# Performance work log

Measured on AMD Instinct MI355X. Metric: run time of the kernel, lower is better.

## Reference

```python
import jax, jax.numpy as jnp
import numpy as np

NUM_HEADS = 16
EPS = 1e-6
ROPE_BASE = 10000.0

def _thw(N, TT):
    table = {2640: (3, 22, 40), 1530: (3, 17, 30), 6120: (3, 34, 60), 660: (3, 11, 20)}
    return table.get(N - TT, (3, 23, 40))

def _positions(t, h, w):
    tt, hh, ww = np.meshgrid(np.arange(t), np.arange(h), np.arange(w), indexing='ij')
    return jnp.asarray(np.stack([tt, hh, ww], -1).reshape(-1, 3), jnp.float32)  # (THW, 3)

def _rope1d(x, pos):
    # x: (B,H,T,d) one axis-chunk, pos: (T,) positions for that axis
    d = x.shape[-1]
    inv_freq = 1.0 / (ROPE_BASE ** (jnp.arange(0, d, 2, dtype=jnp.float32) / d))
    ang = pos[:, None] * inv_freq                     # (T, d/2)
    cos = jnp.concatenate([jnp.cos(ang)] * 2, -1)     # (T, d)
    sin = jnp.concatenate([jnp.sin(ang)] * 2, -1)
    x1, x2 = x[..., : d // 2], x[..., d // 2:]
    return x * cos + jnp.concatenate([-x2, x1], -1) * sin

def _rope3d(x, pos, TT):
    # first TT tokens (text) pass through; video tokens get per-axis rotation
    pre, vid = x[:, :, :TT], x[:, :, TT:]
    chunks = jnp.split(vid, 3, axis=-1)               # t/h/w axis chunks
    rot = [_rope1d(c, pos[:, i]) for i, c in enumerate(chunks)]
    return jnp.concatenate([pre, jnp.concatenate(rot, -1)], axis=2)

def _rms(x, w):
    return x * jax.lax.rsqrt(jnp.mean(x * x, -1, keepdims=True) + EPS) * w

def setup_inputs() -> dict:
    key = jax.random.key(0)
    ks = jax.random.split(key, 12)
    B, N, C = 1, 2866, 1536
    Dh = C // NUM_HEADS
    s = 0.02
    return {
        'x': jax.random.normal(ks[0], (B, N, C), jnp.float32),
        'Wq': jax.random.normal(ks[1], (C, C), jnp.float32) * s,
        'bq': jnp.zeros((C,), jnp.float32),
        'Wk': jax.random.normal(ks[2], (C, C), jnp.float32) * s,
        'bk': jnp.zeros((C,), jnp.float32),
        'Wv': jax.random.normal(ks[3], (C, C), jnp.float32) * s,
        'bv': jnp.zeros((C,), jnp.float32),
        'qn_w': jnp.ones((Dh,), jnp.float32),
        'kn_w': jnp.ones((Dh,), jnp.float32),
        'Wp': jax.random.normal(ks[4], (C, C), jnp.float32) * s,
        'bp': jnp.zeros((C,), jnp.float32),
        'TT': 226,
    }

def reference(x, Wq, bq, Wk, bk, Wv, bv, qn_w, kn_w, Wp, bp, TT):
    B, N, C = x.shape
    H = NUM_HEADS
    Dh = C // H
    def proj(W, b):
        return (x @ W.T + b).reshape(B, N, H, Dh).transpose(0, 2, 1, 3)  # (B,H,N,Dh)
    q, k, v = proj(Wq, bq), proj(Wk, bk), proj(Wv, bv)
    q, k = _rms(q, qn_w), _rms(k, kn_w)
    t, h, w = _thw(N, TT)
    pos = _positions(t, h, w)
    q = _rope3d(q, pos, TT)
    k = _rope3d(k, pos, TT)
    scale = Dh ** -0.5
    attn = jax.nn.softmax(jnp.einsum('bhqd,bhkd->bhqk', q, k) * scale, axis=-1)
    o = jnp.einsum('bhqk,bhkd->bhqd', attn, v)
    o = o.transpose(0, 2, 1, 3).reshape(B, N, C)
    return o @ Wp.T + bp
```

## Files before the change

kernel.cpp:

```cpp
#include <hip/hip_runtime.h>
#include <hip/hip_bf16.h>
#include <math.h>

#define C_DIM 1536
#define H_NUM 16
#define DH    96

typedef __attribute__((ext_vector_type(4))) float  f32x4;
typedef __attribute__((ext_vector_type(8))) short  bf16x8;

__device__ __forceinline__ unsigned short f2bf_rne(float f) {
    unsigned u = __float_as_uint(f);
    unsigned r = (u + 0x7FFFu + ((u >> 16) & 1u)) >> 16;
    return (unsigned short)r;
}
__device__ __forceinline__ float bf2f(unsigned short h) {
    return __uint_as_float(((unsigned)h) << 16);
}

__device__ __forceinline__ void glds16(const void* g, void* l) {
    __builtin_amdgcn_global_load_lds(
        (const __attribute__((address_space(1))) unsigned int*)g,
        (__attribute__((address_space(3))) unsigned int*)l, 16, 0, 0);
}

struct CvtAll {
    const float* src[5];
    unsigned short* hi[5];
    unsigned short* lo[5];
};
__global__ __launch_bounds__(256)
void cvt_all(CvtAll a, int n4x, int n4w)
{
    const int role = blockIdx.y;
    const int n4   = (role == 0) ? n4x : n4w;
    const int i    = blockIdx.x * 256 + threadIdx.x;
    if (i >= n4) return;
    float4 v = *(const float4*)&a.src[role][4 * i];
    unsigned short h[4], l[4];
    float vv[4] = {v.x, v.y, v.z, v.w};
    #pragma unroll
    for (int j = 0; j < 4; ++j) {
        h[j] = f2bf_rne(vv[j]);
        l[j] = f2bf_rne(vv[j] - bf2f(h[j]));
    }
    *(ushort4*)&a.hi[role][4 * i] = *(ushort4*)h;
    *(ushort4*)&a.lo[role][4 * i] = *(ushort4*)l;
}

__global__ __launch_bounds__(256)
void gemm_mfma(const unsigned short* __restrict__ Ahi,
               const unsigned short* __restrict__ Alo,
               const unsigned short* W0h, const unsigned short* W0l,
               const float* b0, float* Y0,
               const unsigned short* W1h, const unsigned short* W1l,
               const float* b1, float* Y1,
               const unsigned short* W2h, const unsigned short* W2l,
               const float* b2, float* Y2,
               int M)
{
    __shared__ __align__(16) unsigned short lds[2 * 4 * 4096];

    const unsigned short* Wh;
    const unsigned short* Wl;
    const float* bias;
    float* Y;
    if (blockIdx.z == 0)      { Wh = W0h; Wl = W0l; bias = b0; Y = Y0; }
    else if (blockIdx.z == 1) { Wh = W1h; Wl = W1l; bias = b1; Y = Y1; }
    else                      { Wh = W2h; Wl = W2l; bias = b2; Y = Y2; }

    const int t   = threadIdx.x;
    const int m0  = blockIdx.x * 128;
    const int n0  = blockIdx.y * 128;
    const int w   = t >> 6;
    const int l   = t & 63;

    const unsigned short* src =
        (w == 0) ? Ahi : (w == 1) ? Alo : (w == 2) ? Wh : Wl;
    const int rbase = (w < 2) ? m0 : n0;
    const int rmax  = (w < 2) ? (M - 1) : 0x3FFFFFFF;
    const int srow  = l >> 2;
    const int scol  = l & 3;
    const int ssw   = (srow >> 1) & 3;
    int goff[8];
    #pragma unroll
    for (int i = 0; i < 8; ++i) {
        int gr = rbase + 16 * i + srow;
        gr = gr < rmax ? gr : rmax;
        goff[i] = gr * C_DIM + 8 * (scol ^ ssw);
    }

    const int lane = t & 63;
    const int wv   = t >> 6;
    const int wm   = wv & 1, wn = wv >> 1;
    const int lrow = lane & 15;
    const int quad = lane >> 4;
    const int pc   = quad ^ ((lrow >> 1) & 3);
    int aoff[4], boff[4];
    #pragma unroll
    for (int i = 0; i < 4; ++i) {
        aoff[i] = (64 * wm + 16 * i + lrow) * 32 + 8 * pc;
        boff[i] = (64 * wn + 16 * i + lrow) * 32 + 8 * pc;
    }

    f32x4 acc[4][4];
    #pragma unroll
    for (int i = 0; i < 4; ++i)
        #pragma unroll
        for (int j = 0; j < 4; ++j) acc[i][j] = (f32x4)0.f;

    #pragma unroll
    for (int i = 0; i < 8; ++i)
        glds16(src + goff[i], (char*)&lds[w * 4096] + i * 1024);

    const int NT = C_DIM / 32;
    for (int kt = 0; kt < NT; ++kt) {
        const int cb = kt & 1;
        const unsigned short* sA = lds + cb * 16384;

        asm volatile("s_waitcnt vmcnt(0)" ::: "memory");
        __builtin_amdgcn_s_barrier();
        __builtin_amdgcn_sched_barrier(0);

        bf16x8 ah[2], al[2], bh[4], bl[4];

        if (kt + 1 < NT) {
            char* dN = (char*)&lds[(cb ^ 1) * 16384 + w * 4096];
            const int k0n = (kt + 1) * 32;
            #pragma unroll
            for (int i = 0; i < 8; ++i)
                glds16(src + goff[i] + k0n, dN + i * 1024);
        }
        #pragma unroll
        for (int j = 0; j < 4; ++j) {
            bh[j] = *(const bf16x8*)&sA[8192 + boff[j]];
            bl[j] = *(const bf16x8*)&sA[12288 + boff[j]];
        }
        #pragma unroll
        for (int i = 0; i < 2; ++i) {
            ah[i] = *(const bf16x8*)&sA[aoff[i]];
            al[i] = *(const bf16x8*)&sA[4096 + aoff[i]];
        }
        __builtin_amdgcn_s_barrier();
        asm volatile("s_waitcnt lgkmcnt(0)" ::: "memory");
        __builtin_amdgcn_sched_barrier(0);
        __builtin_amdgcn_s_setprio(1);
        #pragma unroll
        for (int i = 0; i < 2; ++i)
            #pragma unroll
            for (int j = 0; j < 4; ++j) {
                acc[i][j] = __builtin_amdgcn_mfma_f32_16x16x32_bf16(ah[i], bh[j], acc[i][j], 0, 0, 0);
                acc[i][j] = __builtin_amdgcn_mfma_f32_16x16x32_bf16(al[i], bh[j], acc[i][j], 0, 0, 0);
                acc[i][j] = __builtin_amdgcn_mfma_f32_16x16x32_bf16(ah[i], bl[j], acc[i][j], 0, 0, 0);
            }
        __builtin_amdgcn_s_setprio(0);
        __builtin_amdgcn_s_barrier();
        __builtin_amdgcn_sched_barrier(0);

        #pragma unroll
        for (int i = 0; i < 2; ++i) {
            ah[i] = *(const bf16x8*)&sA[aoff[2 + i]];
            al[i] = *(const bf16x8*)&sA[4096 + aoff[2 + i]];
        }
        __builtin_amdgcn_s_barrier();
        asm volatile("s_waitcnt lgkmcnt(0)" ::: "memory");
        __builtin_amdgcn_sched_barrier(0);
        __builtin_amdgcn_s_setprio(1);
        #pragma unroll
        for (int i = 0; i < 2; ++i)
            #pragma unroll
            for (int j = 0; j < 4; ++j) {
                acc[2 + i][j] = __builtin_amdgcn_mfma_f32_16x16x32_bf16(ah[i], bh[j], acc[2 + i][j], 0, 0, 0);
                acc[2 + i][j] = __builtin_amdgcn_mfma_f32_16x16x32_bf16(al[i], bh[j], acc[2 + i][j], 0, 0, 0);
                acc[2 + i][j] = __builtin_amdgcn_mfma_f32_16x16x32_bf16(ah[i], bl[j], acc[2 + i][j], 0, 0, 0);
            }
        __builtin_amdgcn_s_setprio(0);
    }

    float bv[4];
    #pragma unroll
    for (int j = 0; j < 4; ++j) bv[j] = bias[n0 + 64 * wn + 16 * j + lrow];
    #pragma unroll
    for (int i = 0; i < 4; ++i) {
        const int rbase2 = m0 + 64 * wm + 16 * i + 4 * quad;
        #pragma unroll
        for (int p = 0; p < 4; ++p) {
            const int row = rbase2 + p;
            if (row >= M) continue;
            #pragma unroll
            for (int j = 0; j < 4; ++j) {
                const int col = n0 + 64 * wn + 16 * j + lrow;
                Y[(size_t)row * C_DIM + col] = acc[i][j][p] + bv[j];
            }
        }
    }
}

__global__ __launch_bounds__(512, 2)
void gemm_mfma256(const unsigned short* __restrict__ Ahi,
                  const unsigned short* __restrict__ Alo,
                  const unsigned short* W0h, const unsigned short* W0l,
                  const float* b0, float* Y0,
                  const unsigned short* W1h, const unsigned short* W1l,
                  const float* b1, float* Y1,
                  const unsigned short* W2h, const unsigned short* W2l,
                  const float* b2, float* Y2,
                  int M)
{
    extern __shared__ __align__(16) unsigned short smem[];

    const unsigned short* Wh;
    const unsigned short* Wl;
    const float* bias;
    float* Y;
    if (blockIdx.z == 0)      { Wh = W0h; Wl = W0l; bias = b0; Y = Y0; }
    else if (blockIdx.z == 1) { Wh = W1h; Wl = W1l; bias = b1; Y = Y1; }
    else                      { Wh = W2h; Wl = W2l; bias = b2; Y = Y2; }

    const int t    = threadIdx.x;
    const int wv   = t >> 6;
    const int lane = t & 63;
    const int m0   = blockIdx.x * 256;
    const int n0   = blockIdx.y * 256;

    const int mat  = wv >> 1;
    const int half = wv & 1;
    const unsigned short* src =
        (mat == 0) ? Ahi : (mat == 1) ? Alo : (mat == 2) ? Wh : Wl;
    const int rbase = (mat < 2) ? m0 : n0;
    const int rmax  = (mat < 2) ? (M - 1) : 0x3FFFFFFF;
    const int srow  = lane >> 2;
    const int scol  = lane & 3;
    const int ssw   = (srow >> 1) & 3;
    int goff[8];
    #pragma unroll
    for (int i = 0; i < 8; ++i) {
        int gr = rbase + half * 128 + 16 * i + srow;
        gr = gr < rmax ? gr : rmax;
        goff[i] = gr * C_DIM + 8 * (scol ^ ssw);
    }
    unsigned short* const dstBase = smem + mat * 8192 + half * 4096;

    const int wm   = wv & 1;
    const int wn   = wv >> 1;
    const int lrow = lane & 15;
    const int quad = lane >> 4;
    const int pc   = quad ^ ((lrow >> 1) & 3);
    int aoff[8], boff[4];
    #pragma unroll
    for (int i = 0; i < 8; ++i)
        aoff[i] = (128 * wm + 16 * i + lrow) * 32 + 8 * pc;
    #pragma unroll
    for (int j = 0; j < 4; ++j)
        boff[j] = (64 * wn + 16 * j + lrow) * 32 + 8 * pc;

    f32x4 acc[8][4];
    #pragma unroll
    for (int i = 0; i < 8; ++i)
        #pragma unroll
        for (int j = 0; j < 4; ++j) acc[i][j] = (f32x4)0.f;

    #pragma unroll
    for (int i = 0; i < 8; ++i)
        glds16(src + goff[i], (char*)dstBase + i * 1024);

    const int NT = C_DIM / 32;
    for (int kt = 0; kt < NT; ++kt) {
        const int cb = kt & 1;
        const unsigned short* sA = smem + cb * 32768;
        unsigned short* dN = dstBase + (cb ^ 1) * 32768;
        const int k0n = (kt + 1) * 32;
        const bool pf = (kt + 1 < NT);

        asm volatile("s_waitcnt vmcnt(0)" ::: "memory");
        __builtin_amdgcn_s_barrier();
        __builtin_amdgcn_sched_barrier(0);

        bf16x8 bh[4], bl[4], ah[2], al[2];

        if (pf) {
            #pragma unroll
            for (int i = 0; i < 4; ++i)
                glds16(src + goff[i] + k0n, (char*)dN + i * 1024);
        }
        #pragma unroll
        for (int j = 0; j < 4; ++j) {
            bh[j] = *(const bf16x8*)&sA[16384 + boff[j]];
            bl[j] = *(const bf16x8*)&sA[24576 + boff[j]];
        }
        #pragma unroll
        for (int i = 0; i < 2; ++i) {
            ah[i] = *(const bf16x8*)&sA[aoff[i]];
            al[i] = *(const bf16x8*)&sA[8192 + aoff[i]];
        }
        __builtin_amdgcn_s_barrier();
        asm volatile("s_waitcnt lgkmcnt(0)" ::: "memory");
        __builtin_amdgcn_sched_barrier(0);
        __builtin_amdgcn_s_setprio(1);
        #pragma unroll
        for (int i = 0; i < 2; ++i)
            #pragma unroll
            for (int j = 0; j < 4; ++j) {
                acc[i][j] = __builtin_amdgcn_mfma_f32_16x16x32_bf16(ah[i], bh[j], acc[i][j], 0, 0, 0);
                acc[i][j] = __builtin_amdgcn_mfma_f32_16x16x32_bf16(al[i], bh[j], acc[i][j], 0, 0, 0);
                acc[i][j] = __builtin_amdgcn_mfma_f32_16x16x32_bf16(ah[i], bl[j], acc[i][j], 0, 0, 0);
            }
        __builtin_amdgcn_s_setprio(0);
        __builtin_amdgcn_s_barrier();
        __builtin_amdgcn_sched_barrier(0);

        if (pf) {
            #pragma unroll
            for (int i = 4; i < 8; ++i)
                glds16(src + goff[i] + k0n, (char*)dN + i * 1024);
        }
        #pragma unroll
        for (int i = 0; i < 2; ++i) {
            ah[i] = *(const bf16x8*)&sA[aoff[2 + i]];
            al[i] = *(const bf16x8*)&sA[8192 + aoff[2 + i]];
        }
        __builtin_amdgcn_s_barrier();
        asm volatile("s_waitcnt lgkmcnt(0)" ::: "memory");
        __builtin_amdgcn_sched_barrier(0);
        __builtin_amdgcn_s_setprio(1);
        #pragma unroll
        for (int i = 0; i < 2; ++i)
            #pragma unroll
            for (int j = 0; j < 4; ++j) {
                acc[2 + i][j] = __builtin_amdgcn_mfma_f32_16x16x32_bf16(ah[i], bh[j], acc[2 + i][j], 0, 0, 0);
                acc[2 + i][j] = __builtin_amdgcn_mfma_f32_16x16x32_bf16(al[i], bh[j], acc[2 + i][j], 0, 0, 0);
                acc[2 + i][j] = __builtin_amdgcn_mfma_f32_16x16x32_bf16(ah[i], bl[j], acc[2 + i][j], 0, 0, 0);
            }
        __builtin_amdgcn_s_setprio(0);
        __builtin_amdgcn_s_barrier();
        __builtin_amdgcn_sched_barrier(0);

        #pragma unroll
        for (int i = 0; i < 2; ++i) {
            ah[i] = *(const bf16x8*)&sA[aoff[4 + i]];
            al[i] = *(const bf16x8*)&sA[8192 + aoff[4 + i]];
        }
        __builtin_amdgcn_s_barrier();
        asm volatile("s_waitcnt lgkmcnt(0)" ::: "memory");
        __builtin_amdgcn_sched_barrier(0);
        __builtin_amdgcn_s_setprio(1);
        #pragma unroll
        for (int i = 0; i < 2; ++i)
            #pragma unroll
            for (int j = 0; j < 4; ++j) {
                acc[4 + i][j] = __builtin_amdgcn_mfma_f32_16x16x32_bf16(ah[i], bh[j], acc[4 + i][j], 0, 0, 0);
                acc[4 + i][j] = __builtin_amdgcn_mfma_f32_16x16x32_bf16(al[i], bh[j], acc[4 + i][j], 0, 0, 0);
                acc[4 + i][j] = __builtin_amdgcn_mfma_f32_16x16x32_bf16(ah[i], bl[j], acc[4 + i][j], 0, 0, 0);
            }
        __builtin_amdgcn_s_setprio(0);
        __builtin_amdgcn_s_barrier();
        __builtin_amdgcn_sched_barrier(0);

        #pragma unroll
        for (int i = 0; i < 2; ++i) {
            ah[i] = *(const bf16x8*)&sA[aoff[6 + i]];
            al[i] = *(const bf16x8*)&sA[8192 + aoff[6 + i]];
        }
        __builtin_amdgcn_s_barrier();
        asm volatile("s_waitcnt lgkmcnt(0)" ::: "memory");
        __builtin_amdgcn_sched_barrier(0);
        __builtin_amdgcn_s_setprio(1);
        #pragma unroll
        for (int i = 0; i < 2; ++i)
            #pragma unroll
            for (int j = 0; j < 4; ++j) {
                acc[6 + i][j] = __builtin_amdgcn_mfma_f32_16x16x32_bf16(ah[i], bh[j], acc[6 + i][j], 0, 0, 0);
                acc[6 + i][j] = __builtin_amdgcn_mfma_f32_16x16x32_bf16(al[i], bh[j], acc[6 + i][j], 0, 0, 0);
                acc[6 + i][j] = __builtin_amdgcn_mfma_f32_16x16x32_bf16(ah[i], bl[j], acc[6 + i][j], 0, 0, 0);
            }
        __builtin_amdgcn_s_setprio(0);
    }

    float bv2[4];
    #pragma unroll
    for (int j = 0; j < 4; ++j) bv2[j] = bias[n0 + 64 * wn + 16 * j + lrow];
    #pragma unroll
    for (int i = 0; i < 8; ++i) {
        const int rbase2 = m0 + 128 * wm + 16 * i + 4 * quad;
        #pragma unroll
        for (int p = 0; p < 4; ++p) {
            const int row = rbase2 + p;
            if (row >= M) continue;
            #pragma unroll
            for (int j = 0; j < 4; ++j) {
                const int col = n0 + 64 * wn + 16 * j + lrow;
                Y[(size_t)row * C_DIM + col] = acc[i][j][p] + bv2[j];
            }
        }
    }
}

__global__ __launch_bounds__(256)
void rms_rope_tv(const float* __restrict__ q, const float* __restrict__ k,
                 const float* __restrict__ V,
                 const float* __restrict__ qw, const float* __restrict__ kw,
                 const int* __restrict__ TTp,
                 unsigned short* __restrict__ qhi, unsigned short* __restrict__ khi,
                 unsigned short* __restrict__ vt,
                 int Ntok, int nKt, int vtStride)
{
    __shared__ unsigned short tile[96 * 72];
    const int halfB = (Ntok * H_NUM + 255) >> 8;

    if ((int)blockIdx.x < 2 * halfB) {
        const int role = blockIdx.x / halfB;
        const int idx  = (blockIdx.x % halfB) * 256 + threadIdx.x;
        if (idx >= Ntok * H_NUM) return;
        const int h = idx & (H_NUM - 1);
        const int n = idx >> 4;

        const float* src = role == 0 ? q : k;
        const float* w   = role == 0 ? qw : kw;
        const float* p   = src + (size_t)n * C_DIM + h * DH;

        float ss = 0.f;
        #pragma unroll
        for (int i = 0; i < DH / 4; ++i) {
            float4 v4 = *(const float4*)&p[4 * i];
            ss += v4.x * v4.x;
            ss += v4.y * v4.y;
            ss += v4.z * v4.z;
            ss += v4.w * v4.w;
        }
        const float r = rsqrtf(ss * (1.0f / DH) + 1e-6f);

        const int TT = *TTp;
        const size_t off = (size_t)n * C_DIM + h * DH;
        const float qscale = 0.14724445f;

        if (n < TT) {
            #pragma unroll
            for (int i = 0; i < DH / 4; ++i) {
                float4 v4 = *(const float4*)&p[4 * i];
                float o[4] = {v4.x * (r * w[4 * i + 0]), v4.y * (r * w[4 * i + 1]),
                              v4.z * (r * w[4 * i + 2]), v4.w * (r * w[4 * i + 3])};
                unsigned short hb[4];
                #pragma unroll
                for (int j = 0; j < 4; ++j)
                    hb[j] = (role == 0) ? f2bf_rne(o[j] * qscale) : f2bf_rne(o[j]);
                if (role == 0) *(ushort4*)&qhi[off + 4 * i] = *(ushort4*)hb;
                else           *(ushort4*)&khi[off + 4 * i] = *(ushort4*)hb;
            }
        } else {
            const int pidx = n - TT;
            const int NTt  = Ntok - TT;
            int hh = 23, ww = 40;
            if      (NTt == 2640) { hh = 22; ww = 40; }
            else if (NTt == 1530) { hh = 17; ww = 30; }
            else if (NTt == 6120) { hh = 34; ww = 60; }
            else if (NTt ==  660) { hh = 11; ww = 20; }
            float pos[3];
            pos[0] = (float)(pidx / (hh * ww));
            pos[1] = (float)((pidx / ww) % hh);
            pos[2] = (float)(pidx % ww);
            #pragma unroll
            for (int c = 0; c < 3; ++c) {
                float xa[16], xb[16];
                #pragma unroll
                for (int g = 0; g < 4; ++g) {
                    float4 va = *(const float4*)&p[32 * c + 4 * g];
                    float4 vb = *(const float4*)&p[32 * c + 16 + 4 * g];
                    xa[4 * g + 0] = va.x * (r * w[32 * c + 4 * g + 0]);
                    xa[4 * g + 1] = va.y * (r * w[32 * c + 4 * g + 1]);
                    xa[4 * g + 2] = va.z * (r * w[32 * c + 4 * g + 2]);
                    xa[4 * g + 3] = va.w * (r * w[32 * c + 4 * g + 3]);
                    xb[4 * g + 0] = vb.x * (r * w[32 * c + 16 + 4 * g + 0]);
                    xb[4 * g + 1] = vb.y * (r * w[32 * c + 16 + 4 * g + 1]);
                    xb[4 * g + 2] = vb.z * (r * w[32 * c + 16 + 4 * g + 2]);
                    xb[4 * g + 3] = vb.w * (r * w[32 * c + 16 + 4 * g + 3]);
                }
                #pragma unroll
                for (int j = 0; j < 16; ++j) {
                    const float invf = exp2f(-0.83048202373f * (float)j);
                    const float ang  = pos[c] * invf;
                    const float cs = cosf(ang), sn = sinf(ang);
                    const float a = xa[j], b = xb[j];
                    xa[j] = a * cs - b * sn;
                    xb[j] = a * sn + b * cs;
                }
                #pragma unroll
                for (int g = 0; g < 4; ++g) {
                    unsigned short hb[4];
                    #pragma unroll
                    for (int j = 0; j < 4; ++j)
                        hb[j] = (role == 0) ? f2bf_rne(xa[4 * g + j] * qscale)
                                            : f2bf_rne(xa[4 * g + j]);
                    if (role == 0) *(ushort4*)&qhi[off + 32 * c + 4 * g] = *(ushort4*)hb;
                    else           *(ushort4*)&khi[off + 32 * c + 4 * g] = *(ushort4*)hb;
                }
                #pragma unroll
                for (int g = 0; g < 4; ++g) {
                    unsigned short hb[4];
                    #pragma unroll
                    for (int j = 0; j < 4; ++j)
                        hb[j] = (role == 0) ? f2bf_rne(xb[4 * g + j] * qscale)
                                            : f2bf_rne(xb[4 * g + j]);
                    if (role == 0) *(ushort4*)&qhi[off + 32 * c + 16 + 4 * g] = *(ushort4*)hb;
                    else           *(ushort4*)&khi[off + 32 * c + 16 + 4 * g] = *(ushort4*)hb;
                }
            }
        }
    } else {
        const int b2 = blockIdx.x - 2 * halfB;
        const int t  = threadIdx.x;
        const int k0 = (b2 % nKt) * 64;
        const int h  = b2 / nKt;

        #pragma unroll
        for (int it = 0; it < 6; ++it) {
            const int idx = t + 256 * it;
            const int key = idx / 24, dg = idx % 24;
            float vv[4] = {0.f, 0.f, 0.f, 0.f};
            if (k0 + key < Ntok)
                *(float4*)vv = *(const float4*)&V[(size_t)(k0 + key) * C_DIM + h * DH + 4 * dg];
            #pragma unroll
            for (int j = 0; j < 4; ++j) tile[(4 * dg + j) * 72 + key] = f2bf_rne(vv[j]);
        }
        __syncthreads();
        #pragma unroll
        for (int it = 0; it < 3; ++it) {
            const int idx = t + 256 * it;
            const int d = idx >> 3, ck = idx & 7;
            *(bf16x8*)&vt[((size_t)h * DH + d) * vtStride + k0 + 8 * ck] =
                *(const bf16x8*)&tile[d * 72 + 8 * ck];
        }
    }
}

__global__ __launch_bounds__(256)
void attn_mfma(const unsigned short* __restrict__ qhi,
               const unsigned short* __restrict__ khi,
               const unsigned short* __restrict__ vt,
               unsigned short* __restrict__ Ohi,
               unsigned short* __restrict__ Olo,
               int Ntok, int nKt, int vtStride)
{
    __shared__ unsigned short ldsK[64 * 96];
    __shared__ unsigned short ldsV[96 * 72];
    __shared__ unsigned short ldsP[64 * 72];
    __shared__ float ldsL[64];

    const int t    = threadIdx.x;
    const int lane = t & 63;
    const int wv   = t >> 6;
    const int lrow = lane & 15;
    const int quad = lane >> 4;

    const int Lb  = blockIdx.x + gridDim.x * blockIdx.y;
    const int xcd = Lb & 7;
    const int jj  = Lb >> 3;
    const int h   = 2 * xcd + (jj >= nKt ? 1 : 0);
    const int q0  = (jj >= nKt ? jj - nKt : jj) * 64;
    const size_t hoff = (size_t)h * DH;

    bf16x8 qh[3];
    {
        const int qr = q0 + wv * 16 + lrow;
        if (qr < Ntok) {
            const size_t base = (size_t)qr * C_DIM + hoff + quad * 8;
            #pragma unroll
            for (int kc = 0; kc < 3; ++kc)
                qh[kc] = *(const bf16x8*)&qhi[base + 32 * kc];
        } else {
            const bf16x8 z = {0,0,0,0,0,0,0,0};
            #pragma unroll
            for (int kc = 0; kc < 3; ++kc) qh[kc] = z;
        }
    }

    const int rK  = t >> 2;
    const int cK  = t & 3;
    const int swK = (rK >> 1) & 3;
    const int swf = (lrow >> 1) & 3;
    const int vd  = t >> 3;
    const int vck = t & 7;

    float lsum = 0.f;
    f32x4 oacc[6];
    #pragma unroll
    for (int dt = 0; dt < 6; ++dt) oacc[dt] = (f32x4)0.f;

    const bf16x8 zv = {0,0,0,0,0,0,0,0};
    bf16x8 pk[3], pv[3];
    #pragma unroll
    for (int it = 0; it < 3; ++it) {
        pk[it] = (rK < Ntok) ? *(const bf16x8*)&khi[(size_t)rK * C_DIM + hoff + 8 * (cK + 4 * it)] : zv;
        pv[it] = *(const bf16x8*)&vt[(hoff + vd + 32 * it) * vtStride + 8 * vck];
    }

    const int pRow = (wv * 16 + lrow) * 72;
    for (int kt = 0; kt < nKt; ++kt) {
        const int k0 = kt * 64;
        __syncthreads();
        #pragma unroll
        for (int it = 0; it < 3; ++it) {
            *(bf16x8*)&ldsK[rK * 96 + 8 * (4 * it + (cK ^ swK))] = pk[it];
            *(bf16x8*)&ldsV[(vd + 32 * it) * 72 + 8 * vck]       = pv[it];
        }
        __syncthreads();

        if (kt + 1 < nKt) {
            const int kn = k0 + 64;
            #pragma unroll
            for (int it = 0; it < 3; ++it) {
                pk[it] = (kn + rK < Ntok) ? *(const bf16x8*)&khi[(size_t)(kn + rK) * C_DIM + hoff + 8 * (cK + 4 * it)] : zv;
                pv[it] = *(const bf16x8*)&vt[(hoff + vd + 32 * it) * vtStride + kn + 8 * vck];
            }
        }

        f32x4 sacc[4];
        #pragma unroll
        for (int mt = 0; mt < 4; ++mt) sacc[mt] = (f32x4)0.f;
        #pragma unroll
        for (int kc = 0; kc < 3; ++kc) {
            #pragma unroll
            for (int mt = 0; mt < 4; ++mt) {
                bf16x8 kb = *(const bf16x8*)&ldsK[(lrow + 16 * mt) * 96 + 8 * (4 * kc + (quad ^ swf))];
                sacc[mt] = __builtin_amdgcn_mfma_f32_16x16x32_bf16(kb, qh[kc], sacc[mt], 0, 0, 0);
            }
        }

        if (kt + 1 < nKt) {
            #pragma unroll
            for (int mt = 0; mt < 4; ++mt) {
                float e[4];
                #pragma unroll
                for (int p = 0; p < 4; ++p) e[p] = exp2f(sacc[mt][p]);
                lsum += (e[0] + e[1]) + (e[2] + e[3]);
                unsigned u0 = __float_as_uint(e[0]) + 0x8000u;
                unsigned u1 = __float_as_uint(e[1]) + 0x8000u;
                unsigned u2 = __float_as_uint(e[2]) + 0x8000u;
                unsigned u3 = __float_as_uint(e[3]) + 0x8000u;
                uint2 pr;
                pr.x = __builtin_amdgcn_perm(u1, u0, 0x07060302u);
                pr.y = __builtin_amdgcn_perm(u3, u2, 0x07060302u);
                *(uint2*)&ldsP[pRow + 16 * mt + 4 * quad] = pr;
            }
        } else {
            const int kq = k0 + 4 * quad;
            #pragma unroll
            for (int mt = 0; mt < 4; ++mt) {
                float e[4];
                #pragma unroll
                for (int p = 0; p < 4; ++p)
                    e[p] = (kq + 16 * mt + p < Ntok) ? exp2f(sacc[mt][p]) : 0.f;
                lsum += (e[0] + e[1]) + (e[2] + e[3]);
                unsigned u0 = __float_as_uint(e[0]) + 0x8000u;
                unsigned u1 = __float_as_uint(e[1]) + 0x8000u;
                unsigned u2 = __float_as_uint(e[2]) + 0x8000u;
                unsigned u3 = __float_as_uint(e[3]) + 0x8000u;
                uint2 pr;
                pr.x = __builtin_amdgcn_perm(u1, u0, 0x07060302u);
                pr.y = __builtin_amdgcn_perm(u3, u2, 0x07060302u);
                *(uint2*)&ldsP[pRow + 16 * mt + 4 * quad] = pr;
            }
        }

        #pragma unroll
        for (int kc2 = 0; kc2 < 2; ++kc2) {
            bf16x8 pa = *(const bf16x8*)&ldsP[pRow + 32 * kc2 + 8 * quad];
            #pragma unroll
            for (int dt = 0; dt < 6; ++dt) {
                bf16x8 vb = *(const bf16x8*)&ldsV[(16 * dt + lrow) * 72 + 32 * kc2 + 8 * quad];
                oacc[dt] = __builtin_amdgcn_mfma_f32_16x16x32_bf16(pa, vb, oacc[dt], 0, 0, 0);
            }
        }
    }

    lsum += __shfl_xor(lsum, 16, 64);
    lsum += __shfl_xor(lsum, 32, 64);
    ldsL[wv * 16 + lrow] = lsum;
    #pragma unroll
    for (int p = 0; p < 4; ++p) {
        const int row = q0 + wv * 16 + quad * 4 + p;
        if (row >= Ntok) continue;
        const float rl = 1.0f / ldsL[wv * 16 + quad * 4 + p];
        const size_t rbase = (size_t)row * C_DIM + hoff + lrow;
        #pragma unroll
        for (int dt = 0; dt < 6; ++dt) {
            const float o = oacc[dt][p] * rl;
            const unsigned short hb = f2bf_rne(o);
            Ohi[rbase + 16 * dt] = hb;
            Olo[rbase + 16 * dt] = f2bf_rne(o - bf2f(hb));
        }
    }
}

extern "C" void kernel_launch(void* const* d_in, const int* in_sizes, int n_in,
                              void* d_out, int out_size, void* d_ws, size_t ws_size,
                              hipStream_t stream)
{
    const float* x   = (const float*)d_in[0];
    const float* Wq  = (const float*)d_in[1];
    const float* bq  = (const float*)d_in[2];
    const float* Wk  = (const float*)d_in[3];
    const float* bk  = (const float*)d_in[4];
    const float* Wv  = (const float*)d_in[5];
    const float* bv  = (const float*)d_in[6];
    const float* qnw = (const float*)d_in[7];
    const float* knw = (const float*)d_in[8];
    const float* Wp  = (const float*)d_in[9];
    const float* bp  = (const float*)d_in[10];
    const int*   TTp = (const int*)d_in[11];

    const int Ntok = in_sizes[0] / C_DIM;
    const int nKt  = (Ntok + 63) / 64;
    const int vtStride = nKt * 64;
    const size_t NC = (size_t)Ntok * C_DIM;
    const size_t CC = (size_t)C_DIM * C_DIM;
    float* out = (float*)d_out;

    static bool s_attr = false;
    if (!s_attr) {
        hipFuncSetAttribute(reinterpret_cast<const void*>(gemm_mfma256),
                            hipFuncAttributeMaxDynamicSharedMemorySize, 131072);
        s_attr = true;
    }

    float*          kbuf = (float*)d_ws;
    float*          vbuf = kbuf + NC;
    unsigned short* xhi  = (unsigned short*)(vbuf + NC);
    unsigned short* xlo  = xhi + NC;
    unsigned short* wsp  = xlo + NC;
    unsigned short* wqh = wsp + 0 * CC, *wql = wsp + 1 * CC;
    unsigned short* wkh = wsp + 2 * CC, *wkl = wsp + 3 * CC;
    unsigned short* wvh = wsp + 4 * CC, *wvl = wsp + 5 * CC;
    unsigned short* wph = wsp + 6 * CC, *wpl = wsp + 7 * CC;
    unsigned short* qhib = wsp + 8 * CC;
    unsigned short* khib = qhib + NC;
    unsigned short* vtb  = khib + NC;
    float*          qbuf = out;
    unsigned short* ohi  = (unsigned short*)kbuf;
    unsigned short* olo  = ohi + NC;

    CvtAll ca;
    ca.src[0] = x;  ca.hi[0] = xhi; ca.lo[0] = xlo;
    ca.src[1] = Wq; ca.hi[1] = wqh; ca.lo[1] = wql;
    ca.src[2] = Wk; ca.hi[2] = wkh; ca.lo[2] = wkl;
    ca.src[3] = Wv; ca.hi[3] = wvh; ca.lo[3] = wvl;
    ca.src[4] = Wp; ca.hi[4] = wph; ca.lo[4] = wpl;
    cvt_all<<<dim3((NC / 4 + 255) / 256, 5), 256, 0, stream>>>(
        ca, (int)(NC / 4), (int)(CC / 4));

    dim3 qkvgrid((Ntok + 255) / 256, C_DIM / 256, 3);
    gemm_mfma256<<<qkvgrid, 512, 131072, stream>>>(xhi, xlo,
        wqh, wql, bq, qbuf,
        wkh, wkl, bk, kbuf,
        wvh, wvl, bv, vbuf, Ntok);

    const int halfB = (Ntok * H_NUM + 255) / 256;
    rms_rope_tv<<<dim3(2 * halfB + nKt * H_NUM), 256, 0, stream>>>(
        qbuf, kbuf, vbuf, qnw, knw, TTp, qhib, khib, vtb, Ntok, nKt, vtStride);

    attn_mfma<<<dim3(nKt, H_NUM), 256, 0, stream>>>(
        qhib, khib, vtb, ohi, olo, Ntok, nKt, vtStride);

    dim3 pgrid((Ntok + 127) / 128, C_DIM / 128, 1);
    gemm_mfma<<<pgrid, 256, 0, stream>>>(ohi, olo,
        wph, wpl, bp, out,
        wph, wpl, bp, out,
        wph, wpl, bp, out, Ntok);
}
```

Baseline: 413.0 us.

## Split attention keys into two partitions with a combine kernel

Splits the key range of attention into two halves launched as a third grid dimension, doubling the block count. Each half writes unnormalized partial outputs (hi/lo bf16) and row sums, and a new combine kernel adds them and normalizes. The aim is better CU occupancy on the attention kernel, since 45x16 blocks is few for the GPU. The cost is extra global traffic for partials and one more launch. This works without a running max because the softmax uses no max subtraction.

```diff
diff --git a/kernel.cpp b/kernel.cpp
--- a/kernel.cpp
+++ b/kernel.cpp
@@ -536,9 +536,10 @@
 void attn_mfma(const unsigned short* __restrict__ qhi,
                const unsigned short* __restrict__ khi,
                const unsigned short* __restrict__ vt,
-               unsigned short* __restrict__ Ohi,
-               unsigned short* __restrict__ Olo,
-               int Ntok, int nKt, int vtStride)
+               unsigned short* __restrict__ S0h, unsigned short* __restrict__ S0l,
+               unsigned short* __restrict__ S1h, unsigned short* __restrict__ S1l,
+               float* __restrict__ lbuf,
+               int Ntok, int nKt, int nK0, int vtStride)
 {
     __shared__ unsigned short ldsK[64 * 96];
     __shared__ unsigned short ldsV[96 * 72];
@@ -550,6 +551,13 @@
     const int wv   = t >> 6;
     const int lrow = lane & 15;
     const int quad = lane >> 4;
+
+    const int part  = blockIdx.z;
+    const int ktBeg = part ? nK0 : 0;
+    const int ktEnd = part ? nKt : nK0;
+    unsigned short* const Shi = part ? S1h : S0h;
+    unsigned short* const Slo = part ? S1l : S0l;
+    float* const lout = lbuf + (size_t)part * Ntok * H_NUM;
 
     const int Lb  = blockIdx.x + gridDim.x * blockIdx.y;
     const int xcd = Lb & 7;
@@ -587,14 +595,15 @@
 
     const bf16x8 zv = {0,0,0,0,0,0,0,0};
     bf16x8 pk[3], pv[3];
+    const int kB = ktBeg * 64;
     #pragma unroll
     for (int it = 0; it < 3; ++it) {
-        pk[it] = (rK < Ntok) ? *(const bf16x8*)&khi[(size_t)rK * C_DIM + hoff + 8 * (cK + 4 * it)] : zv;
-        pv[it] = *(const bf16x8*)&vt[(hoff + vd + 32 * it) * vtStride + 8 * vck];
+        pk[it] = (kB + rK < Ntok) ? *(const bf16x8*)&khi[(size_t)(kB + rK) * C_DIM + hoff + 8 * (cK + 4 * it)] : zv;
+        pv[it] = *(const bf16x8*)&vt[(hoff + vd + 32 * it) * vtStride + kB + 8 * vck];
     }
 
     const int pRow = (wv * 16 + lrow) * 72;
-    for (int kt = 0; kt < nKt; ++kt) {
+    for (int kt = ktBeg; kt < ktEnd; ++kt) {
         const int k0 = kt * 64;
         __syncthreads();
         #pragma unroll
@@ -604,7 +613,7 @@
         }
         __syncthreads();
 
-        if (kt + 1 < nKt) {
+        if (kt + 1 < ktEnd) {
             const int kn = k0 + 64;
             #pragma unroll
             for (int it = 0; it < 3; ++it) {
@@ -625,7 +634,7 @@
             }
         }
 
-        if (kt + 1 < nKt) {
+        if (kt != nKt - 1) {
             #pragma unroll
             for (int mt = 0; mt < 4; ++mt) {
                 float e[4];
@@ -679,16 +688,53 @@
     for (int p = 0; p < 4; ++p) {
         const int row = q0 + wv * 16 + quad * 4 + p;
         if (row >= Ntok) continue;
-        const float rl = 1.0f / ldsL[wv * 16 + quad * 4 + p];
+        if (lrow == 0)
+            lout[(size_t)row * H_NUM + h] = ldsL[wv * 16 + quad * 4 + p];
         const size_t rbase = (size_t)row * C_DIM + hoff + lrow;
         #pragma unroll
         for (int dt = 0; dt < 6; ++dt) {
-            const float o = oacc[dt][p] * rl;
+            const float o = oacc[dt][p];
             const unsigned short hb = f2bf_rne(o);
-            Ohi[rbase + 16 * dt] = hb;
-            Olo[rbase + 16 * dt] = f2bf_rne(o - bf2f(hb));
-        }
-    }
+            Shi[rbase + 16 * dt] = hb;
+            Slo[rbase + 16 * dt] = f2bf_rne(o - bf2f(hb));
+        }
+    }
+}
+
+__global__ __launch_bounds__(256)
+void attn_combine(const unsigned short* __restrict__ s0h, const unsigned short* __restrict__ s0l,
+                  const unsigned short* __restrict__ s1h, const unsigned short* __restrict__ s1l,
+                  const float* __restrict__ lbuf,
+                  unsigned short* __restrict__ ohi, unsigned short* __restrict__ olo,
+                  int Ntok)
+{
+    const int i  = blockIdx.x * 256 + threadIdx.x;
+    const int n4 = Ntok * (C_DIM / 4);
+    if (i >= n4) return;
+    const int row = (4 * i) / C_DIM;
+    const int col = (4 * i) % C_DIM;
+    const int h   = col / DH;
+    const float rl = 1.0f /
+        (lbuf[(size_t)row * H_NUM + h] + lbuf[(size_t)Ntok * H_NUM + (size_t)row * H_NUM + h]);
+
+    ushort4 a0 = *(const ushort4*)&s0h[4 * i];
+    ushort4 b0 = *(const ushort4*)&s0l[4 * i];
+    ushort4 a1 = *(const ushort4*)&s1h[4 * i];
+    ushort4 b1 = *(const ushort4*)&s1l[4 * i];
+    const unsigned short* pa0 = (const unsigned short*)&a0;
+    const unsigned short* pb0 = (const unsigned short*)&b0;
+    const unsigned short* pa1 = (const unsigned short*)&a1;
+    const unsigned short* pb1 = (const unsigned short*)&b1;
+    unsigned short oh[4], ol[4];
+    #pragma unroll
+    for (int j = 0; j < 4; ++j) {
+        const float s = (bf2f(pa0[j]) + bf2f(pb0[j])) + (bf2f(pa1[j]) + bf2f(pb1[j]));
+        const float o = s * rl;
+        oh[j] = f2bf_rne(o);
+        ol[j] = f2bf_rne(o - bf2f(oh[j]));
+    }
+    *(ushort4*)&ohi[4 * i] = *(ushort4*)oh;
+    *(ushort4*)&olo[4 * i] = *(ushort4*)ol;
 }
 
 extern "C" void kernel_launch(void* const* d_in, const int* in_sizes, int n_in,
@@ -710,6 +756,7 @@
 
     const int Ntok = in_sizes[0] / C_DIM;
     const int nKt  = (Ntok + 63) / 64;
+    const int nK0  = (nKt + 1) / 2;
     const int vtStride = nKt * 64;
     const size_t NC = (size_t)Ntok * C_DIM;
     const size_t CC = (size_t)C_DIM * C_DIM;
@@ -734,9 +781,14 @@
     unsigned short* qhib = wsp + 8 * CC;
     unsigned short* khib = qhib + NC;
     unsigned short* vtb  = khib + NC;
+    float*          lbuf = (float*)(vtb + (size_t)H_NUM * DH * vtStride);
     float*          qbuf = out;
-    unsigned short* ohi  = (unsigned short*)kbuf;
-    unsigned short* olo  = ohi + NC;
+    unsigned short* s0h = (unsigned short*)kbuf;
+    unsigned short* s0l = s0h + NC;
+    unsigned short* s1h = (unsigned short*)vbuf;
+    unsigned short* s1l = s1h + NC;
+    unsigned short* ohi = xhi;
+    unsigned short* olo = xlo;
 
     CvtAll ca;
     ca.src[0] = x;  ca.hi[0] = xhi; ca.lo[0] = xlo;
@@ -757,8 +809,11 @@
     rms_rope_tv<<<dim3(2 * halfB + nKt * H_NUM), 256, 0, stream>>>(
         qbuf, kbuf, vbuf, qnw, knw, TTp, qhib, khib, vtb, Ntok, nKt, vtStride);
 
-    attn_mfma<<<dim3(nKt, H_NUM), 256, 0, stream>>>(
-        qhib, khib, vtb, ohi, olo, Ntok, nKt, vtStride);
+    attn_mfma<<<dim3(nKt, H_NUM, 2), 256, 0, stream>>>(
+        qhib, khib, vtb, s0h, s0l, s1h, s1l, lbuf, Ntok, nKt, nK0, vtStride);
+
+    attn_combine<<<dim3((NC / 4 + 255) / 256), 256, 0, stream>>>(
+        s0h, s0l, s1h, s1l, lbuf, ohi, olo, Ntok);
 
     dim3 pgrid((Ntok + 127) / 128, C_DIM / 128, 1);
     gemm_mfma<<<pgrid, 256, 0, stream>>>(ohi, olo,
```

Measured after the change: 421.2 us. About the same (+2.0%).
